# Kernel tuning notes

Measured on AMD Instinct MI355X. Metric: run time of the kernel, lower is better.

Reference implementation:

```python
import jax, jax.numpy as jnp
import numpy as np

B, N, D = 4, 2048, 1024
H, A, Lv = 8, 128, 128   # heads, attention_dim (qk), linear_dim (v)
NUM_BLOCKS = 4
QKV_W = (2 * Lv + 2 * A) * H  # 4096
NEG = -1e9


def setup_inputs() -> dict:
    key = jax.random.key(0)
    ks = jax.random.split(key, 10)
    past_lengths = jax.random.randint(ks[0], (B,), 0, N)
    past_ids = jax.random.randint(ks[1], (B, N), 0, 10000)
    past_embeddings = jax.random.normal(ks[2], (B, N, D), dtype=jnp.float32)
    # per-block parameters, stacked on leading block axis (xavier-ish scale)
    qkv_w = jax.random.normal(ks[3], (NUM_BLOCKS, D, QKV_W), dtype=jnp.float32) * (1.0 / np.sqrt(D))
    qkv_b = jnp.zeros((NUM_BLOCKS, QKV_W), dtype=jnp.float32)
    out_w = jax.random.normal(ks[4], (NUM_BLOCKS, Lv * H, D), dtype=jnp.float32) * (1.0 / np.sqrt(Lv * H))
    out_b = jnp.zeros((NUM_BLOCKS, D), dtype=jnp.float32)
    ln_g = jnp.ones((NUM_BLOCKS, D), dtype=jnp.float32)
    ln_b = jnp.zeros((NUM_BLOCKS, D), dtype=jnp.float32)
    return {"past_lengths": past_lengths, "past_ids": past_ids,
            "past_embeddings": past_embeddings, "qkv_w": qkv_w, "qkv_b": qkv_b,
            "out_w": out_w, "out_b": out_b, "ln_g": ln_g, "ln_b": ln_b}


def _layer_norm(x, g, b, eps=1e-5):
    mu = jnp.mean(x, axis=-1, keepdims=True)
    var = jnp.mean(jnp.square(x - mu), axis=-1, keepdims=True)
    return (x - mu) * jax.lax.rsqrt(var + eps) * g + b


def _block(x, mask, qw, qb, ow, ob, g, b):
    xn = _layer_norm(x, g, b)
    qkv = (xn @ qw + qb).reshape(B, N, H, 2 * Lv + 2 * A)
    q = qkv[..., :A]              # [B,N,H,A]
    k = qkv[..., A:2 * A]         # [B,N,H,A]
    v = qkv[..., 2 * A:2 * A + Lv]  # [B,N,H,Lv]
    scores = jnp.einsum('bnha,bmha->bhnm', q, k) / np.sqrt(A)
    # original: masked_fill(-inf) -> silu -> /N -> softmax; we mask after the
    # silu transform with a large-negative logit so masked weights are ~0
    logits = jnp.where(mask[:, None, :, :], jax.nn.silu(scores) / N, NEG)
    w = jax.nn.softmax(logits, axis=-1)
    attn = jnp.einsum('bhnm,bmhl->bnhl', w, v).reshape(B, N, H * Lv)
    return x + attn @ ow + ob


def reference(past_lengths, past_ids, past_embeddings, qkv_w, qkv_b, out_w, out_b, ln_g, ln_b):
    valid = past_ids != 0                                   # [B,N]
    causal = jnp.triu(jnp.ones((N, N), dtype=bool), k=1)     # faithful to buffer (triu, diag=1)
    mask = causal[None] & valid[:, None, :] & valid[:, :, None]  # [B,N,N]
    x = past_embeddings
    for i in range(NUM_BLOCKS):
        x = _block(x, mask, qkv_w[i], qkv_b[i], out_w[i], out_b[i], ln_g[i], ln_b[i])
    return x
```

## Files before the change

### kernel.cpp

```cpp
#include <hip/hip_runtime.h>

typedef __bf16 bf16_t;
typedef __bf16 bf16x8 __attribute__((ext_vector_type(8)));
typedef __bf16 bf16x4 __attribute__((ext_vector_type(4)));
typedef float f32x4 __attribute__((ext_vector_type(4)));

#define B_ 4
#define N_ 2048
#define D_ 1024
#define H_ 8
#define NB_ 4
#define M_ (B_*N_)
#define QN_ 3072
#define QKN_ 2048

__device__ __forceinline__ void async_copy16(const void* gsrc, void* ldst) {
    __builtin_amdgcn_global_load_lds(
        (const __attribute__((address_space(1))) void*)gsrc,
        (__attribute__((address_space(3))) void*)ldst, 16, 0, 0);
}

static constexpr size_t WT_OFF  = 0;
static constexpr size_t WT_SZ   = (size_t)NB_*QN_*D_*2;
static constexpr size_t OWT_OFF = WT_OFF + WT_SZ;
static constexpr size_t OWT_SZ  = (size_t)NB_*D_*D_*2;
static constexpr size_t XN_OFF  = OWT_OFF + OWT_SZ;
static constexpr size_t XN_SZ   = (size_t)M_*D_*2;
static constexpr size_t QK_OFF  = XN_OFF + XN_SZ;
static constexpr size_t QK_SZ   = (size_t)M_*QKN_*2;
static constexpr size_t VT_OFF  = QK_OFF + QK_SZ;
static constexpr size_t VT_SZ   = (size_t)32*128*N_*2;
static constexpr size_t ATT_OFF = VT_OFF + VT_SZ;
static constexpr size_t ATT_SZ  = (size_t)M_*D_*2;
static constexpr size_t QBR_OFF = ATT_OFF + ATT_SZ;
static constexpr size_t QBR_SZ  = (size_t)NB_*QN_*4;
static constexpr size_t VS_OFF  = QBR_OFF + QBR_SZ;

__global__ __launch_bounds__(256) void repack_qkvw(const float* __restrict__ qw, bf16_t* __restrict__ wt)
{
    __shared__ float tile[64][65];
    const int nb = blockIdx.z;
    const int j0 = blockIdx.x * 64, d0 = blockIdx.y * 64;
    const int tx = threadIdx.x, ty = threadIdx.y;
    const float* src = qw + (size_t)nb * D_ * 4096;
    const int jj = j0 + tx;
    const int sel = jj >> 10, rr = jj & 1023, hh = rr >> 7, aa = rr & 127;
    const int orig = hh * 512 + sel * 128 + aa;
#pragma unroll
    for (int it = 0; it < 16; ++it) {
        int dr = it * 4 + ty;
        tile[dr][tx] = src[(size_t)(d0 + dr) * 4096 + orig];
    }
    __syncthreads();
    bf16_t* dst = wt + (size_t)nb * QN_ * D_;
#pragma unroll
    for (int it = 0; it < 16; ++it) {
        int jr = it * 4 + ty;
        dst[(size_t)(j0 + jr) * D_ + d0 + tx] = (bf16_t)tile[tx][jr];
    }
}

__global__ __launch_bounds__(256) void repack_outw(const float* __restrict__ ow, bf16_t* __restrict__ owt)
{
    __shared__ float tile[64][65];
    const int nb = blockIdx.z;
    const int j0 = blockIdx.x * 64, d0 = blockIdx.y * 64;
    const int tx = threadIdx.x, ty = threadIdx.y;
    const float* src = ow + (size_t)nb * D_ * D_;
#pragma unroll
    for (int it = 0; it < 16; ++it) {
        int dr = it * 4 + ty;
        tile[dr][tx] = src[(size_t)(d0 + dr) * D_ + j0 + tx];
    }
    __syncthreads();
    bf16_t* dst = owt + (size_t)nb * D_ * D_;
#pragma unroll
    for (int it = 0; it < 16; ++it) {
        int jr = it * 4 + ty;
        dst[(size_t)(j0 + jr) * D_ + d0 + tx] = (bf16_t)tile[tx][jr];
    }
}

__global__ __launch_bounds__(256) void repack_qb(const float* __restrict__ qb, float* __restrict__ qbr)
{
    int idx = blockIdx.x * 256 + threadIdx.x;
    int nb = idx / QN_, jj = idx % QN_;
    int sel = jj >> 10, rr = jj & 1023, hh = rr >> 7, aa = rr & 127;
    qbr[idx] = qb[nb * 4096 + hh * 512 + sel * 128 + aa];
}

__global__ __launch_bounds__(256) void ln_kernel(const float* __restrict__ x, const float* __restrict__ g,
                                                 const float* __restrict__ bb, bf16_t* __restrict__ xn)
{
    const int row = blockIdx.x, tid = threadIdx.x;
    const float4 v = ((const float4*)(x + (size_t)row * D_))[tid];
    float s = v.x + v.y + v.z + v.w;
    float q = v.x * v.x + v.y * v.y + v.z * v.z + v.w * v.w;
#pragma unroll
    for (int d = 32; d >= 1; d >>= 1) { s += __shfl_xor(s, d); q += __shfl_xor(q, d); }
    __shared__ float ls[4], lq[4];
    if ((tid & 63) == 0) { ls[tid >> 6] = s; lq[tid >> 6] = q; }
    __syncthreads();
    s = ls[0] + ls[1] + ls[2] + ls[3];
    q = lq[0] + lq[1] + lq[2] + lq[3];
    const float mean = s * (1.f / 1024.f);
    const float var  = q * (1.f / 1024.f) - mean * mean;
    const float inv  = rsqrtf(var + 1e-5f);
    const float4 gg = ((const float4*)g)[tid];
    const float4 bv = ((const float4*)bb)[tid];
    bf16x4 o;
    o[0] = (bf16_t)((v.x - mean) * inv * gg.x + bv.x);
    o[1] = (bf16_t)((v.y - mean) * inv * gg.y + bv.y);
    o[2] = (bf16_t)((v.z - mean) * inv * gg.z + bv.z);
    o[3] = (bf16_t)((v.w - mean) * inv * gg.w + bv.w);
    *(bf16x4*)(xn + (size_t)row * D_ + tid * 4) = o;
}

template<bool RESID>
__global__ __launch_bounds__(512, 2) void gemm256(const bf16_t* __restrict__ Am, const bf16_t* __restrict__ Bt,
                                                  const float* __restrict__ bias, float* __restrict__ resid_out,
                                                  bf16_t* __restrict__ outH, bf16_t* __restrict__ vtOut,
                                                  int Kn, int Nn, int vSplit)
{
    __shared__ bf16_t As[4 * 256 * 32];
    __shared__ bf16_t Bs[4 * 128 * 32];
    const int tid = threadIdx.x;
    const int lane = tid & 63, wave = tid >> 6;
    const int wr = wave >> 2, wc = wave & 3;
    const int quad = lane >> 4, l15 = lane & 15;
    const int swz = quad ^ ((l15 >> 1) & 3);
    const int slane8 = ((lane & 3) ^ ((lane >> 3) & 3)) * 8;
    const int lrow = lane >> 2;
    const int m0 = blockIdx.y * 256, n0 = blockIdx.x * 128;

    const int chA0 = wave * 2, chA1 = chA0 + 1;
    const bf16_t* gA0 = Am + (size_t)(m0 + chA0 * 16 + lrow) * Kn + slane8;
    const bf16_t* gA1 = Am + (size_t)(m0 + chA1 * 16 + lrow) * Kn + slane8;
    const bf16_t* gB  = Bt + (size_t)(n0 + wave * 16 + lrow) * Kn + slane8;
    bf16_t* const dA0 = &As[chA0 * 512];
    bf16_t* const dA1 = &As[chA1 * 512];
    bf16_t* const dB  = &Bs[wave * 512];

    auto STAGE = [&](int slot) {
        async_copy16(gA0, dA0 + slot * 8192);
        async_copy16(gA1, dA1 + slot * 8192);
        async_copy16(gB,  dB  + slot * 4096);
        gA0 += 32; gA1 += 32; gB += 32;
    };

    f32x4 acc[8][2] = {};
    const int NT = Kn >> 5;

    STAGE(0); STAGE(1); STAGE(2);
    asm volatile("s_waitcnt vmcnt(6)" ::: "memory");
    __builtin_amdgcn_s_barrier();

    const int aoff = (wr * 128 + l15) * 32 + swz * 8;
    const int boff = (wc * 32  + l15) * 32 + swz * 8;

    for (int t = 0; t < NT; ++t) {
        const int ring = t & 3;
        const bf16_t* ra = &As[ring * 8192 + aoff];
        const bf16_t* rb = &Bs[ring * 4096 + boff];
        bf16x8 af[8], bfv[2];
#pragma unroll
        for (int i = 0; i < 8; ++i) af[i] = *(const bf16x8*)(ra + i * 512);
#pragma unroll
        for (int j = 0; j < 2; ++j) bfv[j] = *(const bf16x8*)(rb + j * 512);
        if (t + 3 < NT) STAGE((t + 3) & 3);
        __builtin_amdgcn_s_barrier();
        asm volatile("s_waitcnt lgkmcnt(0)" ::: "memory");
        __builtin_amdgcn_s_setprio(1);
#pragma unroll
        for (int i = 0; i < 8; ++i)
#pragma unroll
            for (int j = 0; j < 2; ++j)
                acc[i][j] = __builtin_amdgcn_mfma_f32_16x16x32_bf16(af[i], bfv[j], acc[i][j], 0, 0, 0);
        __builtin_amdgcn_s_setprio(0);
        if (t + 3 < NT)      asm volatile("s_waitcnt vmcnt(6)" ::: "memory");
        else if (t + 2 < NT) asm volatile("s_waitcnt vmcnt(3)" ::: "memory");
        else if (t + 1 < NT) asm volatile("s_waitcnt vmcnt(0)" ::: "memory");
        __builtin_amdgcn_s_barrier();
    }

    if (!RESID && n0 >= vSplit) {
#pragma unroll
        for (int i = 0; i < 8; ++i) {
            const int rowg = m0 + wr * 128 + i * 16 + quad * 4;
            const int bb2 = rowg >> 11, mloc = rowg & 2047;
            const int mperm = (mloc & ~31) | (((mloc >> 2) & 3) << 3) | (((mloc >> 4) & 1) << 2);
#pragma unroll
            for (int j = 0; j < 2; ++j) {
                const int colg = n0 + wc * 32 + j * 16 + l15;
                const int hh = (colg - 2048) >> 7, ll = (colg - 2048) & 127;
                const float bv = bias[colg];
                bf16x4 sv;
#pragma unroll
                for (int r = 0; r < 4; ++r) sv[r] = (bf16_t)(acc[i][j][r] + bv);
                *(bf16x4*)(vtOut + ((size_t)(bb2 * 8 + hh) * 128 + ll) * (size_t)N_ + mperm) = sv;
            }
        }
        return;
    }
#pragma unroll
    for (int i = 0; i < 8; ++i) {
#pragma unroll
        for (int j = 0; j < 2; ++j) {
            const int colg = n0 + wc * 32 + j * 16 + l15;
            const float bv = bias[colg];
#pragma unroll
            for (int r = 0; r < 4; ++r) {
                const int rowg = m0 + wr * 128 + i * 16 + quad * 4 + r;
                const size_t off = (size_t)rowg * Nn + colg;
                const float v = acc[i][j][r] + bv;
                if (RESID) resid_out[off] += v;
                else       outH[off] = (bf16_t)v;
            }
        }
    }
}

__global__ __launch_bounds__(256) void vsum_kernel(const bf16_t* __restrict__ vt, float* __restrict__ vs)
{
    const int gid = blockIdx.x * 4 + (threadIdx.x >> 6);
    const int lane = threadIdx.x & 63;
    const bf16_t* p = vt + (size_t)gid * N_ + lane * 8;
    float s = 0.f;
#pragma unroll
    for (int c = 0; c < 4; ++c) {
        bf16x8 v = *(const bf16x8*)(p + c * 512);
#pragma unroll
        for (int u = 0; u < 8; ++u) s += (float)v[u];
    }
#pragma unroll
    for (int d = 32; d >= 1; d >>= 1) s += __shfl_xor(s, d);
    if (lane == 0) vs[gid] = s;
}

template<bool CAUSAL>
__device__ __forceinline__ void attn_tile(
    int m0, int m0n, int n0, int b, int h,
    const bf16_t* __restrict__ qk, const bf16_t* __restrict__ vtb,
    bf16_t* Ks, bf16_t* Vs, const unsigned int* mb,
    const bf16x8 (&qf)[2][4], bf16x8 onesf, float vnf0, float vnf1,
    f32x4 (&oacc)[2][8], f32x4 (&dacc)[2])
{
    const int tid = threadIdx.x, lane = tid & 63, wave = tid >> 6;
    const int quad = lane >> 4, l15 = lane & 15;
    const int swz = quad ^ ((l15 >> 1) & 3);
    const int slane8 = ((lane & 3) ^ ((lane >> 3) & 3)) * 8;
    const int lrow = lane >> 2;
    const float scaleA = 0.08838834764831845f;
    const float invN = 1.f / 2048.f;

#pragma unroll
    for (int s = 0; s < 8; ++s) {
        const int kkc = s & 3, rg = (s >> 2) + wave * 2;
        async_copy16(vtb + (size_t)(rg * 16 + lrow) * N_ + m0 + kkc * 32 + slane8,
                     &Vs[kkc * 4096 + rg * 512 + lane * 8]);
    }

    f32x4 sacc[2][8] = {};
    __builtin_amdgcn_s_setprio(1);
#pragma unroll
    for (int kk = 0; kk < 4; ++kk) {
#pragma unroll
        for (int j = 0; j < 8; ++j) {
            bf16x8 kf = *(const bf16x8*)&Ks[kk * 4096 + (j * 16 + l15) * 32 + swz * 8];
            sacc[0][j] = __builtin_amdgcn_mfma_f32_16x16x32_bf16(kf, qf[0][kk], sacc[0][j], 0, 0, 0);
            sacc[1][j] = __builtin_amdgcn_mfma_f32_16x16x32_bf16(kf, qf[1][kk], sacc[1][j], 0, 0, 0);
        }
    }
    __builtin_amdgcn_s_setprio(0);

    unsigned int wj[4];
#pragma unroll
    for (int q = 0; q < 4; ++q) wj[q] = mb[(m0 >> 5) + q];
    bf16x8 pf[2][4];
#pragma unroll
    for (int kk = 0; kk < 4; ++kk) {
#pragma unroll
        for (int s = 0; s < 2; ++s) {
            const int j = kk * 2 + s;
            const unsigned int wrd = wj[j >> 1];
            const int shl = (j & 1) * 16 + quad * 4;
#pragma unroll
            for (int nb = 0; nb < 2; ++nb) {
                const float vn = nb ? vnf1 : vnf0;
#pragma unroll
                for (int r = 0; r < 4; ++r) {
                    const float sv = sacc[nb][j][r] * scaleA;
                    const float xc = fminf(fmaxf(sv, -4.f), 4.f);
                    float sig = __builtin_fmaf(xc, 0.25f, 0.5f);
                    sig = __builtin_fmaf(-(xc * 0.03125f), fabsf(xc), sig);
                    float e = __builtin_fmaf(sv * sig, invN, 1.f);
                    e = ((wrd >> (shl + r)) & 1) ? e * vn : 0.f;
                    if (CAUSAL) {
                        const int dmn = (m0 + j * 16 + quad * 4 + r) - (n0 + wave * 32 + nb * 16 + l15);
                        e = (dmn > 0) ? e : 0.f;
                    }
                    pf[nb][kk][s * 4 + r] = (bf16_t)e;
                }
            }
        }
    }

    __syncthreads();

    if (m0n < N_) {
        const size_t baseq = (size_t)b * N_ * QKN_;
#pragma unroll
        for (int s = 0; s < 8; ++s) {
            const int kkc = s & 3, rg = (s >> 2) + wave * 2;
            async_copy16(qk + baseq + (size_t)(m0n + rg * 16 + lrow) * QKN_ + 1024 + h * 128 + kkc * 32 + slane8,
                         &Ks[kkc * 4096 + rg * 512 + lane * 8]);
        }
    }

    __builtin_amdgcn_s_setprio(1);
#pragma unroll
    for (int kk = 0; kk < 4; ++kk) {
        dacc[0] = __builtin_amdgcn_mfma_f32_16x16x32_bf16(pf[0][kk], onesf, dacc[0], 0, 0, 0);
        dacc[1] = __builtin_amdgcn_mfma_f32_16x16x32_bf16(pf[1][kk], onesf, dacc[1], 0, 0, 0);
#pragma unroll
        for (int j = 0; j < 8; ++j) {
            bf16x8 vf = *(const bf16x8*)&Vs[kk * 4096 + (j * 16 + l15) * 32 + swz * 8];
            oacc[0][j] = __builtin_amdgcn_mfma_f32_16x16x32_bf16(pf[0][kk], vf, oacc[0][j], 0, 0, 0);
            oacc[1][j] = __builtin_amdgcn_mfma_f32_16x16x32_bf16(pf[1][kk], vf, oacc[1][j], 0, 0, 0);
        }
    }
    __builtin_amdgcn_s_setprio(0);
    __syncthreads();
}

__global__ __launch_bounds__(256, 2) void attn_kernel(const bf16_t* __restrict__ qk, const bf16_t* __restrict__ vt,
                                                      const int* __restrict__ past_ids, const float* __restrict__ vsum,
                                                      bf16_t* __restrict__ att)
{
    __shared__ bf16_t Ks[4 * 128 * 32];
    __shared__ bf16_t Vs[4 * 128 * 32];
    __shared__ unsigned long long mbits[32];

    const int bx = blockIdx.x;
    const int bh = bx & 31, g = bx >> 5;
    const int t = (g < 8) ? g : 23 - g;
    const int b = bh >> 3, h = bh & 7;
    const int n0 = t << 7;
    const int tid = threadIdx.x, lane = tid & 63, wave = tid >> 6;
    const int quad = lane >> 4, l15 = lane & 15;
    const int slane8 = ((lane & 3) ^ ((lane >> 3) & 3)) * 8;
    const int lrow = lane >> 2;
    const bf16_t* vtb = vt + (size_t)bh * 128 * N_;
    const float invN = 1.f / 2048.f;

#pragma unroll
    for (int it = 0; it < 8; ++it) {
        const int m = (wave * 8 + it) * 64 + lane;
        const unsigned long long bal = __ballot(past_ids[b * N_ + m] != 0);
        if (lane == 0) mbits[wave * 8 + it] = bal;
    }

    bf16x8 qf[2][4];
#pragma unroll
    for (int nb = 0; nb < 2; ++nb) {
        const bf16_t* gq = qk + (size_t)b * N_ * QKN_ + (size_t)(n0 + wave * 32 + nb * 16 + l15) * QKN_ + h * 128 + quad * 8;
#pragma unroll
        for (int kk = 0; kk < 4; ++kk) qf[nb][kk] = *(const bf16x8*)(gq + kk * 32);
    }
    const float vnf0 = past_ids[b * N_ + n0 + wave * 32 + l15] != 0 ? 1.f : 0.f;
    const float vnf1 = past_ids[b * N_ + n0 + wave * 32 + 16 + l15] != 0 ? 1.f : 0.f;
    bf16x8 onesf;
#pragma unroll
    for (int i = 0; i < 8; ++i) onesf[i] = (bf16_t)1.f;

    {
        const size_t baseq = (size_t)b * N_ * QKN_;
#pragma unroll
        for (int s = 0; s < 8; ++s) {
            const int kkc = s & 3, rg = (s >> 2) + wave * 2;
            async_copy16(qk + baseq + (size_t)(n0 + rg * 16 + lrow) * QKN_ + 1024 + h * 128 + kkc * 32 + slane8,
                         &Ks[kkc * 4096 + rg * 512 + lane * 8]);
        }
    }
    __syncthreads();

    f32x4 oacc[2][8] = {};
    f32x4 dacc[2] = {};
    const unsigned int* mb = (const unsigned int*)mbits;

    attn_tile<true>(n0, n0 + 128, n0, b, h, qk, vtb, Ks, Vs, mb, qf, onesf, vnf0, vnf1, oacc, dacc);
    for (int m0 = n0 + 128; m0 < N_; m0 += 128)
        attn_tile<false>(m0, m0 + 128, n0, b, h, qk, vtb, Ks, Vs, mb, qf, onesf, vnf0, vnf1, oacc, dacc);

    float vsr[8];
#pragma unroll
    for (int j = 0; j < 8; ++j) vsr[j] = vsum[bh * 128 + j * 16 + l15];
#pragma unroll
    for (int nb = 0; nb < 2; ++nb) {
#pragma unroll
        for (int r = 0; r < 4; ++r) {
            const float dn = dacc[nb][r];
            const bool uni = !(dn > 0.f);
            const float rc = uni ? 0.f : __builtin_amdgcn_rcpf(dn);
            const int gn = n0 + wave * 32 + nb * 16 + quad * 4 + r;
#pragma unroll
            for (int j = 0; j < 8; ++j) {
                const float ov = uni ? (vsr[j] * invN) : (oacc[nb][j][r] * rc);
                att[(size_t)(b * N_ + gn) * 1024 + h * 128 + j * 16 + l15] = (bf16_t)ov;
            }
        }
    }
}

extern "C" void kernel_launch(void* const* d_in, const int* in_sizes, int n_in,
                              void* d_out, int out_size, void* d_ws, size_t ws_size,
                              hipStream_t stream) {
    (void)in_sizes; (void)n_in; (void)out_size; (void)ws_size;
    const int*   past_ids = (const int*)d_in[1];
    const float* past_emb = (const float*)d_in[2];
    const float* qkv_w    = (const float*)d_in[3];
    const float* qkv_b    = (const float*)d_in[4];
    const float* out_w    = (const float*)d_in[5];
    const float* out_b    = (const float*)d_in[6];
    const float* ln_g     = (const float*)d_in[7];
    const float* ln_b     = (const float*)d_in[8];

    float* x = (float*)d_out;
    char* ws = (char*)d_ws;
    bf16_t* WT  = (bf16_t*)(ws + WT_OFF);
    bf16_t* OWT = (bf16_t*)(ws + OWT_OFF);
    bf16_t* XN  = (bf16_t*)(ws + XN_OFF);
    bf16_t* QK  = (bf16_t*)(ws + QK_OFF);
    bf16_t* VT  = (bf16_t*)(ws + VT_OFF);
    bf16_t* ATT = (bf16_t*)(ws + ATT_OFF);
    float*  QBR = (float*)(ws + QBR_OFF);
    float*  VS  = (float*)(ws + VS_OFF);

    hipMemcpyAsync(x, past_emb, (size_t)M_ * D_ * sizeof(float), hipMemcpyDeviceToDevice, stream);
    repack_qkvw<<<dim3(48, 16, NB_), dim3(64, 4), 0, stream>>>(qkv_w, WT);
    repack_outw<<<dim3(16, 16, NB_), dim3(64, 4), 0, stream>>>(out_w, OWT);
    repack_qb<<<48, 256, 0, stream>>>(qkv_b, QBR);

    for (int layer = 0; layer < NB_; ++layer) {
        ln_kernel<<<M_, 256, 0, stream>>>(x, ln_g + layer * D_, ln_b + layer * D_, XN);
        gemm256<false><<<dim3(QN_ / 128, M_ / 256), 512, 0, stream>>>(
            XN, WT + (size_t)layer * QN_ * D_, QBR + layer * QN_, nullptr, QK, VT, D_, QKN_, 2048);
        vsum_kernel<<<1024, 256, 0, stream>>>(VT, VS);
        attn_kernel<<<512, 256, 0, stream>>>(QK, VT, past_ids, VS, ATT);
        gemm256<true><<<dim3(D_ / 128, M_ / 256), 512, 0, stream>>>(
            ATT, OWT + (size_t)layer * D_ * D_, out_b + layer * D_, x, nullptr, nullptr, D_, D_, 1 << 30);
    }
}
```

Before: 923.4 us.

## Add dedicated 256x256-tile QKV GEMM kernel with block-uniform V-transpose epilogue

Introduces a specialized QKV projection GEMM that uses 256x256 output tiles instead of 256x128. This raises arithmetic intensity per loaded byte and halves the number of blocks. Because each 256-column tile lies wholly in either the QK or the V region, the V-transpose branch is uniform across the block. The larger tile doubles LDS use and accumulator registers per thread (128 floats), which may cut occupancy or cause spills, and the grid of 12x32 blocks may fill the CUs less evenly.

```diff
diff --git a/kernel.cpp b/kernel.cpp
--- a/kernel.cpp
+++ b/kernel.cpp
@@ -116,6 +116,107 @@
     *(bf16x4*)(xn + (size_t)row * D_ + tid * 4) = o;
 }
 
+__global__ __launch_bounds__(512, 2) void gemm_qkv(const bf16_t* __restrict__ Am, const bf16_t* __restrict__ Bt,
+                                                   const float* __restrict__ bias,
+                                                   bf16_t* __restrict__ outQK, bf16_t* __restrict__ vtOut)
+{
+    __shared__ bf16_t As[4 * 8192];
+    __shared__ bf16_t Bs[4 * 8192];
+    const int tid = threadIdx.x;
+    const int lane = tid & 63, wave = tid >> 6;
+    const int wr = wave >> 2, wc = wave & 3;
+    const int quad = lane >> 4, l15 = lane & 15;
+    const int swz = quad ^ ((l15 >> 1) & 3);
+    const int slane8 = ((lane & 3) ^ ((lane >> 3) & 3)) * 8;
+    const int lrow = lane >> 2;
+    const int m0 = blockIdx.y * 256, n0 = blockIdx.x * 256;
+    const int Kn = D_;
+
+    const int ch = wave * 2;
+    const bf16_t* gA0 = Am + (size_t)(m0 + ch * 16 + lrow) * Kn + slane8;
+    const bf16_t* gA1 = gA0 + (size_t)16 * Kn;
+    const bf16_t* gB0 = Bt + (size_t)(n0 + ch * 16 + lrow) * Kn + slane8;
+    const bf16_t* gB1 = gB0 + (size_t)16 * Kn;
+    bf16_t* const dA0 = &As[ch * 512 + lane * 8];
+    bf16_t* const dA1 = &As[(ch + 1) * 512 + lane * 8];
+    bf16_t* const dB0 = &Bs[ch * 512 + lane * 8];
+    bf16_t* const dB1 = &Bs[(ch + 1) * 512 + lane * 8];
+
+    auto STAGE = [&](int slot) {
+        async_copy16(gA0, dA0 + slot * 8192);
+        async_copy16(gA1, dA1 + slot * 8192);
+        async_copy16(gB0, dB0 + slot * 8192);
+        async_copy16(gB1, dB1 + slot * 8192);
+        gA0 += 32; gA1 += 32; gB0 += 32; gB1 += 32;
+    };
+
+    f32x4 acc[8][4] = {};
+    const int NT = Kn >> 5;
+
+    STAGE(0); STAGE(1); STAGE(2);
+    asm volatile("s_waitcnt vmcnt(8)" ::: "memory");
+    __builtin_amdgcn_s_barrier();
+
+    const int aoff = wr * 4096 + l15 * 32 + swz * 8;
+    const int boff = wc * 2048 + l15 * 32 + swz * 8;
+
+    for (int t = 0; t < NT; ++t) {
+        const int ring = t & 3;
+        const bf16_t* ra = &As[ring * 8192 + aoff];
+        const bf16_t* rb = &Bs[ring * 8192 + boff];
+        bf16x8 af[8], bfv[4];
+#pragma unroll
+        for (int j = 0; j < 4; ++j) bfv[j] = *(const bf16x8*)(rb + j * 512);
+#pragma unroll
+        for (int i = 0; i < 8; ++i) af[i] = *(const bf16x8*)(ra + i * 512);
+        if (t + 3 < NT) STAGE((t + 3) & 3);
+        __builtin_amdgcn_s_setprio(1);
+#pragma unroll
+        for (int i = 0; i < 8; ++i)
+#pragma unroll
+            for (int j = 0; j < 4; ++j)
+                acc[i][j] = __builtin_amdgcn_mfma_f32_16x16x32_bf16(af[i], bfv[j], acc[i][j], 0, 0, 0);
+        __builtin_amdgcn_s_setprio(0);
+        if (t + 3 < NT)      asm volatile("s_waitcnt vmcnt(8)" ::: "memory");
+        else if (t + 2 < NT) asm volatile("s_waitcnt vmcnt(4)" ::: "memory");
+        else if (t + 1 < NT) asm volatile("s_waitcnt vmcnt(0)" ::: "memory");
+        __builtin_amdgcn_s_barrier();
+    }
+
+    if (n0 >= 2048) {
+#pragma unroll
+        for (int i = 0; i < 8; ++i) {
+            const int rowg = m0 + wr * 128 + i * 16 + quad * 4;
+            const int bb2 = rowg >> 11, mloc = rowg & 2047;
+            const int mperm = (mloc & ~31) | (((mloc >> 2) & 3) << 3) | (((mloc >> 4) & 1) << 2);
+#pragma unroll
+            for (int j = 0; j < 4; ++j) {
+                const int colg = n0 + wc * 64 + j * 16 + l15;
+                const int hh = (colg - 2048) >> 7, ll = (colg - 2048) & 127;
+                const float bv = bias[colg];
+                bf16x4 sv;
+#pragma unroll
+                for (int r = 0; r < 4; ++r) sv[r] = (bf16_t)(acc[i][j][r] + bv);
+                *(bf16x4*)(vtOut + ((size_t)(bb2 * 8 + hh) * 128 + ll) * (size_t)N_ + mperm) = sv;
+            }
+        }
+        return;
+    }
+#pragma unroll
+    for (int i = 0; i < 8; ++i) {
+#pragma unroll
+        for (int j = 0; j < 4; ++j) {
+            const int colg = n0 + wc * 64 + j * 16 + l15;
+            const float bv = bias[colg];
+#pragma unroll
+            for (int r = 0; r < 4; ++r) {
+                const int rowg = m0 + wr * 128 + i * 16 + quad * 4 + r;
+                outQK[(size_t)rowg * QKN_ + colg] = (bf16_t)(acc[i][j][r] + bv);
+            }
+        }
+    }
+}
+
 template<bool RESID>
 __global__ __launch_bounds__(512, 2) void gemm256(const bf16_t* __restrict__ Am, const bf16_t* __restrict__ Bt,
                                                   const float* __restrict__ bias, float* __restrict__ resid_out,
@@ -443,8 +544,8 @@
 
     for (int layer = 0; layer < NB_; ++layer) {
         ln_kernel<<<M_, 256, 0, stream>>>(x, ln_g + layer * D_, ln_b + layer * D_, XN);
-        gemm256<false><<<dim3(QN_ / 128, M_ / 256), 512, 0, stream>>>(
-            XN, WT + (size_t)layer * QN_ * D_, QBR + layer * QN_, nullptr, QK, VT, D_, QKN_, 2048);
+        gemm_qkv<<<dim3(QN_ / 256, M_ / 256), 512, 0, stream>>>(
+            XN, WT + (size_t)layer * QN_ * D_, QBR + layer * QN_, QK, VT);
         vsum_kernel<<<1024, 256, 0, stream>>>(VT, VS);
         attn_kernel<<<512, 256, 0, stream>>>(QK, VT, past_ids, VS, ATT);
         gemm256<true><<<dim3(D_ / 128, M_ / 256), 512, 0, stream>>>(
```

New measurement: 893.0 us. 3.3% less time.
